# Kernel tuning notes

Hardware: AMD Instinct MI355X
Metric: run time of the kernel (lower is better)

Reference implementation:

```python
import jax, jax.numpy as jnp
import numpy as np

B = 1024
E = 200          # entity_dim (== relation_dim)
R = 200          # relation_dim
NE = 50000       # num_entities
NR = 400         # num_relations
OC = 32          # out_channels
FW = 9           # filt_w (filt_h = 1)
WP = E - FW + 1  # conv output width = 192
FC_IN = OC * WP  # 6144
EPS = 1e-5


def setup_inputs() -> dict:
    key = jax.random.key(0)
    ks = jax.random.split(key, 20)
    s = lambda n: 1.0 / np.sqrt(n)
    inp = {
        "e_s": jax.random.randint(ks[0], (B,), 0, NE, dtype=jnp.int32),
        "q_s": jax.random.randint(ks[1], (B,), 0, NR, dtype=jnp.int32),
        "e_c": jax.random.randint(ks[2], (B,), 0, NE, dtype=jnp.int32),
        "entity_emb": jax.random.normal(ks[3], (NE, E), jnp.float32) * 0.1,
        "relation_emb": jax.random.normal(ks[4], (NR, R), jnp.float32) * 0.1,
        "W1_w": jax.random.normal(ks[5], (E + R, R), jnp.float32) * s(E + R),
        "W1_b": jnp.zeros((R,), jnp.float32),
        "fc1_w": jax.random.normal(ks[6], (R, OC * FW), jnp.float32) * s(R),
        "fc1_b": jnp.zeros((OC * FW,), jnp.float32),
        "fc_w": jax.random.normal(ks[7], (FC_IN, E), jnp.float32) * s(FC_IN),
        "fc_b": jnp.zeros((E,), jnp.float32),
        "bn0_g": jnp.ones((1,), jnp.float32),
        "bn0_b": jnp.zeros((1,), jnp.float32),
        "bn0_m": jnp.zeros((1,), jnp.float32),
        "bn0_v": jnp.ones((1,), jnp.float32),
        "bn1_g": jnp.ones((OC,), jnp.float32),
        "bn1_b": jnp.zeros((OC,), jnp.float32),
        "bn1_m": jnp.zeros((OC,), jnp.float32),
        "bn1_v": jnp.ones((OC,), jnp.float32),
        "bn2_g": jnp.ones((E,), jnp.float32),
        "bn2_b": jnp.zeros((E,), jnp.float32),
        "bn2_m": jnp.zeros((E,), jnp.float32),
        "bn2_v": jnp.ones((E,), jnp.float32),
        "bias_b": jnp.zeros((NE,), jnp.float32),
    }
    return inp


def reference(e_s, q_s, e_c, entity_emb, relation_emb, W1_w, W1_b,
              fc1_w, fc1_b, fc_w, fc_b,
              bn0_g, bn0_b, bn0_m, bn0_v,
              bn1_g, bn1_b, bn1_m, bn1_v,
              bn2_g, bn2_b, bn2_m, bn2_v, bias_b):
    es = entity_emb[e_s]                      # [B,E]
    ec = entity_emb[e_c]                      # [B,E]
    r = relation_emb[q_s]                     # [B,R]
    # W1: Linear(E+R -> R); here R == E so e1 has width E
    e1 = jnp.concatenate([es, ec], -1) @ W1_w + W1_b          # [B,E]
    # bn0: single channel, inference mode
    x = (e1 - bn0_m) * (bn0_g / jnp.sqrt(bn0_v + EPS)) + bn0_b  # [B,E]
    # per-sample dynamic filters from fc1(r)
    k = (r @ fc1_w + fc1_b).reshape(B, OC, FW)                # [B,OC,FW]
    # grouped conv (groups=B) == per-sample 1D sliding dot products
    patches = jnp.stack([x[:, w:w + WP] for w in range(FW)], axis=-1)  # [B,WP,FW]
    conv = jnp.einsum('bpw,bow->bop', patches, k)             # [B,OC,WP]
    # bn1 over the OC channel, inference mode
    conv = (conv - bn1_m[:, None]) * (bn1_g / jnp.sqrt(bn1_v + EPS))[:, None] + bn1_b[:, None]
    flat = conv.reshape(B, FC_IN)                             # [B, OC*WP]
    h = flat @ fc_w + fc_b                                    # [B,E]
    h = (h - bn2_m) * (bn2_g / jnp.sqrt(bn2_v + EPS)) + bn2_b
    h = jax.nn.relu(h)
    logits = h @ entity_emb.T + bias_b                        # [B,NE]
    return jax.nn.sigmoid(logits)
```

## Files before the change

### kernel.cpp

```cpp
#include <hip/hip_runtime.h>

#define B_   1024
#define E_   200
#define NE_  50000
#define OC_  32
#define FW_  9
#define WP_  192
#define FCIN 6144
#define CATK 400
#define KDIM 288

typedef __attribute__((ext_vector_type(8))) short short8;
typedef __attribute__((ext_vector_type(4))) float floatx4;
typedef __attribute__((ext_vector_type(4))) unsigned short ushort4v;

static __device__ __forceinline__ float bf2f(unsigned short u) {
  return __uint_as_float(((unsigned)u) << 16);
}
static __device__ __forceinline__ unsigned short f2bf(float f) {
  unsigned u = __float_as_uint(f);
  u += 0x7FFFu + ((u >> 16) & 1u);
  return (unsigned short)(u >> 16);
}

#define PREP_CVT_BLKS   9766
#define PREP_GATH_BLKS  2400
#define PREP_W1_BLKS    28
#define PREP_FC1_BLKS   20
#define PREP_FCW_BLKS   384
#define PREP_R1 (PREP_CVT_BLKS)
#define PREP_R2 (PREP_R1 + PREP_GATH_BLKS)
#define PREP_R3 (PREP_R2 + PREP_W1_BLKS)
#define PREP_R4 (PREP_R3 + PREP_FC1_BLKS)
#define PREP_TOTAL (PREP_R4 + PREP_FCW_BLKS)

static __device__ __forceinline__ void transpose_region(
    const float* __restrict__ in, unsigned short* __restrict__ out,
    int N, int Npad, int K, int bx, int by,
    unsigned short (*lds)[65]) {
  int n0 = bx * 64, k0 = by * 64;
  int tx = threadIdx.x & 63, ty = threadIdx.x >> 6;
#pragma unroll
  for (int kk = 0; kk < 16; kk++) {
    int k = k0 + ty + 4 * kk;
    int n = n0 + tx;
    unsigned short v = 0;
    if (k < K && n < N) v = f2bf(in[(long)k * N + n]);
    lds[ty + 4 * kk][tx] = v;
  }
  __syncthreads();
#pragma unroll
  for (int kk = 0; kk < 16; kk++) {
    int k = k0 + tx;
    int n = n0 + ty + 4 * kk;
    if (n < Npad && k < K) out[(long)n * K + k] = lds[tx][ty + 4 * kk];
  }
}

__global__ __launch_bounds__(256) void k_prep(
    const float* __restrict__ ent, const float* __restrict__ rel,
    const int* __restrict__ e_s, const int* __restrict__ q_s, const int* __restrict__ e_c,
    const float* __restrict__ W1w, const float* __restrict__ fc1w, const float* __restrict__ fcw,
    unsigned short* __restrict__ entb, unsigned short* __restrict__ cat,
    unsigned short* __restrict__ rbuf, unsigned short* __restrict__ W1T,
    unsigned short* __restrict__ fc1T, unsigned short* __restrict__ fcwT) {
  __shared__ unsigned short lds[64][65];
  int blk = blockIdx.x, tid = threadIdx.x;
  if (blk < PREP_R1) {
    int i = blk * 256 + tid;
    if (i < NE_ * E_ / 4) {
      float4 v = ((const float4*)ent)[i];
      ushort4v o = {f2bf(v.x), f2bf(v.y), f2bf(v.z), f2bf(v.w)};
      ((ushort4v*)entb)[i] = o;
    }
  } else if (blk < PREP_R2) {
    int idx = (blk - PREP_R1) * 256 + tid;
    if (idx < B_ * CATK) {
      int s = idx / CATK, i = idx - s * CATK;
      int row = (i < E_) ? e_s[s] : e_c[s];
      int col = (i < E_) ? i : i - E_;
      cat[idx] = f2bf(ent[row * E_ + col]);
    } else {
      int j = idx - B_ * CATK;
      int s = j / E_, i = j - s * E_;
      rbuf[j] = f2bf(rel[q_s[s] * E_ + i]);
    }
  } else if (blk < PREP_R3) {
    int l = blk - PREP_R2;
    transpose_region(W1w, W1T, 200, 208, CATK, l % 4, l / 4, lds);
  } else if (blk < PREP_R4) {
    int l = blk - PREP_R3;
    transpose_region(fc1w, fc1T, 288, 288, E_, l % 5, l / 5, lds);
  } else {
    int l = blk - PREP_R4;
    transpose_region(fcw, fcwT, 200, 208, FCIN, l % 4, l / 4, lds);
  }
}

template<int NK, int RQ>
static __device__ __forceinline__ floatx4 gemm_64x16(
    const unsigned short* __restrict__ A, int lda,
    const unsigned short* __restrict__ Bt, int ldb, int m0, int n0) {
  int lane = threadIdx.x & 63;
  int wv   = threadIdx.x >> 6;
  int l16  = lane & 15, quad = lane >> 4;
  const unsigned short* ap = A  + (long)(m0 + 16 * wv + l16) * lda + quad * 8;
  const unsigned short* bp = Bt + (long)(n0 + l16) * ldb + quad * 8;
  floatx4 acc = {0.f, 0.f, 0.f, 0.f};
#pragma unroll 4
  for (int ks = 0; ks < NK; ks++) {
    short8 a = *(const short8*)(ap + ks * 32);
    short8 b = *(const short8*)(bp + ks * 32);
    acc = __builtin_amdgcn_mfma_f32_16x16x32_bf16(a, b, acc, 0, 0, 0);
  }
  if (RQ > 0) {
    short8 z = {0,0,0,0,0,0,0,0};
    short8 a = (quad < RQ) ? *(const short8*)(ap + NK * 32) : z;
    short8 b = (quad < RQ) ? *(const short8*)(bp + NK * 32) : z;
    acc = __builtin_amdgcn_mfma_f32_16x16x32_bf16(a, b, acc, 0, 0, 0);
  }
  return acc;
}

__global__ __launch_bounds__(256) void k_gemm_ek(
    const unsigned short* __restrict__ cat, const unsigned short* __restrict__ W1T,
    const float* __restrict__ W1b,
    const float* __restrict__ g0, const float* __restrict__ b0,
    const float* __restrict__ m0p, const float* __restrict__ v0,
    unsigned short* __restrict__ xbuf,
    const unsigned short* __restrict__ rbuf, const unsigned short* __restrict__ fc1T,
    const float* __restrict__ fc1b,
    const float* __restrict__ g1, const float* __restrict__ v1,
    unsigned short* __restrict__ kbuf) {
  int blk = blockIdx.x;
  int lane = threadIdx.x & 63, wv = threadIdx.x >> 6;
  int l16 = lane & 15, quad = lane >> 4;
  if (blk < 208) {
    int m0 = (blk & 15) * 64, n0 = (blk >> 4) * 16;
    floatx4 acc = gemm_64x16<12, 2>(cat, CATK, W1T, CATK, m0, n0);
    int j = n0 + l16;
    if (j < E_) {
      float s0  = g0[0] * rsqrtf(v0[0] + 1e-5f);
      float off = (W1b[j] - m0p[0]) * s0 + b0[0];
      int rbase = m0 + 16 * wv + quad * 4;
#pragma unroll
      for (int i = 0; i < 4; i++)
        xbuf[(rbase + i) * E_ + j] = f2bf(acc[i] * s0 + off);
    }
  } else {
    int l = blk - 208;
    int m0 = (l & 15) * 64, n0 = (l >> 4) * 16;
    floatx4 acc = gemm_64x16<6, 1>(rbuf, E_, fc1T, E_, m0, n0);
    int c = n0 + l16;
    int o = c / FW_;
    float s1 = g1[o] * rsqrtf(v1[o] + 1e-5f);
    float fb = fc1b[c];
    int rbase = m0 + 16 * wv + quad * 4;
#pragma unroll
    for (int i = 0; i < 4; i++)
      kbuf[(rbase + i) * KDIM + c] = f2bf((acc[i] + fb) * s1);
  }
}

__global__ __launch_bounds__(256) void k_conv(
    const unsigned short* __restrict__ xbuf, const unsigned short* __restrict__ kbuf,
    const float* __restrict__ g1, const float* __restrict__ b1,
    const float* __restrict__ m1, const float* __restrict__ v1,
    unsigned short* __restrict__ flat) {
  __shared__ float xs[E_];
  __shared__ float ks[KDIM];
  __shared__ float beta[OC_];
  int b = blockIdx.x, tid = threadIdx.x;
  if (tid < E_)  xs[tid] = bf2f(xbuf[b * E_ + tid]);
  for (int i = tid; i < KDIM; i += 256) ks[i] = bf2f(kbuf[b * KDIM + i]);
  if (tid < OC_) {
    float s = g1[tid] * rsqrtf(v1[tid] + 1e-5f);
    beta[tid] = b1[tid] - m1[tid] * s;
  }
  __syncthreads();
  int o = tid >> 3, pc = tid & 7;
  int p0 = pc * 24;
  float kw[FW_];
#pragma unroll
  for (int w = 0; w < FW_; w++) kw[w] = ks[o * FW_ + w];
  float xw[32];
#pragma unroll
  for (int q = 0; q < 8; q++) {
    float4 v = *(const float4*)&xs[p0 + 4 * q];
    xw[4 * q + 0] = v.x; xw[4 * q + 1] = v.y; xw[4 * q + 2] = v.z; xw[4 * q + 3] = v.w;
  }
  float bo = beta[o];
  unsigned short* fp = flat + b * FCIN + o * WP_ + p0;
#pragma unroll
  for (int j = 0; j < 24; j += 2) {
    float a0 = bo, a1 = bo;
#pragma unroll
    for (int w = 0; w < FW_; w++) {
      a0 += xw[j + w] * kw[w];
      a1 += xw[j + 1 + w] * kw[w];
    }
    unsigned pack = (unsigned)f2bf(a0) | ((unsigned)f2bf(a1) << 16);
    *(unsigned*)(fp + j) = pack;
  }
}

__global__ __launch_bounds__(256) void k_gemm_fc(
    const unsigned short* __restrict__ flat, const unsigned short* __restrict__ fcwT,
    float* __restrict__ partial) {
  int m0 = blockIdx.x * 64, n0 = blockIdx.y * 16, kc = blockIdx.z;
  int lane = threadIdx.x & 63, wv = threadIdx.x >> 6;
  int l16 = lane & 15, quad = lane >> 4;
  const unsigned short* ap = flat + (long)(m0 + 16 * wv + l16) * FCIN + kc * 768 + quad * 8;
  const unsigned short* bp = fcwT + (long)(n0 + l16) * FCIN + kc * 768 + quad * 8;
  floatx4 acc = {0.f, 0.f, 0.f, 0.f};
#pragma unroll 4
  for (int ks = 0; ks < 24; ks++) {
    short8 a = *(const short8*)(ap + ks * 32);
    short8 b = *(const short8*)(bp + ks * 32);
    acc = __builtin_amdgcn_mfma_f32_16x16x32_bf16(a, b, acc, 0, 0, 0);
  }
  int j = n0 + l16;
  int rbase = m0 + 16 * wv + quad * 4;
#pragma unroll
  for (int i = 0; i < 4; i++)
    partial[((long)kc * B_ + rbase + i) * 208 + j] = acc[i];
}

__global__ __launch_bounds__(256) void k_fc_epi(
    const float* __restrict__ partial, const float* __restrict__ fcb,
    const float* __restrict__ g2, const float* __restrict__ b2,
    const float* __restrict__ m2, const float* __restrict__ v2,
    unsigned short* __restrict__ hbuf) {
  int idx = blockIdx.x * 256 + threadIdx.x;
  if (idx >= B_ * E_) return;
  int m = idx / E_, j = idx - m * E_;
  float s = 0.f;
#pragma unroll
  for (int kc = 0; kc < 8; kc++) s += partial[((long)kc * B_ + m) * 208 + j];
  float s2 = g2[j] * rsqrtf(v2[j] + 1e-5f);
  float h = (s + fcb[j] - m2[j]) * s2 + b2[j];
  hbuf[idx] = f2bf(fmaxf(h, 0.f));
}

__global__ __launch_bounds__(512, 4) void k_gemm_out(
    const unsigned short* __restrict__ hbuf, const unsigned short* __restrict__ entb,
    const float* __restrict__ bias, float* __restrict__ out) {
  __shared__ __align__(16) unsigned short Blds[7 * 4 * 128 * 8];
  int g = blockIdx.x;
  int xcd = g & 7, local_ = g >> 3;
  int T = (xcd < 4 ? xcd * 196 : 784 + (xcd - 4) * 195) + local_;
  int mt = T & 3, nt = T >> 2;
  int m0 = mt * 256, n0 = nt * 128;
  int tid = threadIdx.x;

#pragma unroll
  for (int it = 0; it < 7; ++it) {
    int idx = it * 512 + tid;
    int ks = idx >> 9, qd = (idx >> 7) & 3, np = idx & 127;
    int col = 8 * (np & 15) + (np >> 4);
    int n = n0 + col;
    int kb = ks * 32 + qd * 8;
    short8 v = {0, 0, 0, 0, 0, 0, 0, 0};
    if (kb < 200 && n < NE_) v = *(const short8*)(entb + (long)n * E_ + kb);
    *(short8*)(Blds + idx * 8) = v;
  }
  __syncthreads();

  int lane = tid & 63, wv = tid >> 6;
  int l16 = lane & 15, quad = lane >> 4;
  const unsigned short* ap0 = hbuf + (long)(m0 + wv * 32 + l16) * E_ + quad * 8;
  const unsigned short* ap1 = ap0 + 16 * E_;

  floatx4 acc[16];
#pragma unroll
  for (int i = 0; i < 16; ++i) acc[i] = (floatx4){0.f, 0.f, 0.f, 0.f};

#pragma unroll
  for (int ks = 0; ks < 6; ++ks) {
    short8 a0 = *(const short8*)(ap0 + ks * 32);
    short8 a1 = *(const short8*)(ap1 + ks * 32);
    const unsigned short* bb = Blds + (ks * 4 + quad) * 1024 + l16 * 8;
#pragma unroll
    for (int nf = 0; nf < 8; ++nf) {
      short8 b = *(const short8*)(bb + nf * 128);
      acc[nf]     = __builtin_amdgcn_mfma_f32_16x16x32_bf16(a0, b, acc[nf], 0, 0, 0);
      acc[8 + nf] = __builtin_amdgcn_mfma_f32_16x16x32_bf16(a1, b, acc[8 + nf], 0, 0, 0);
    }
  }
  {
    short8 z = {0, 0, 0, 0, 0, 0, 0, 0};
    short8 a0 = (quad == 0) ? *(const short8*)(ap0 + 192) : z;
    short8 a1 = (quad == 0) ? *(const short8*)(ap1 + 192) : z;
    const unsigned short* bb = Blds + (24 + quad) * 1024 + l16 * 8;
#pragma unroll
    for (int nf = 0; nf < 8; ++nf) {
      short8 b = *(const short8*)(bb + nf * 128);
      acc[nf]     = __builtin_amdgcn_mfma_f32_16x16x32_bf16(a0, b, acc[nf], 0, 0, 0);
      acc[8 + nf] = __builtin_amdgcn_mfma_f32_16x16x32_bf16(a1, b, acc[8 + nf], 0, 0, 0);
    }
  }

  int nb = n0 + 8 * l16;
  if (nb >= NE_) return;
  float4 bi0 = *(const float4*)(bias + nb);
  float4 bi1 = *(const float4*)(bias + nb + 4);
#pragma unroll
  for (int mf = 0; mf < 2; ++mf) {
#pragma unroll
    for (int i = 0; i < 4; ++i) {
      int row = m0 + wv * 32 + mf * 16 + quad * 4 + i;
      float4 v0, v1;
      v0.x = 1.f / (1.f + __expf(-(acc[mf * 8 + 0][i] + bi0.x)));
      v0.y = 1.f / (1.f + __expf(-(acc[mf * 8 + 1][i] + bi0.y)));
      v0.z = 1.f / (1.f + __expf(-(acc[mf * 8 + 2][i] + bi0.z)));
      v0.w = 1.f / (1.f + __expf(-(acc[mf * 8 + 3][i] + bi0.w)));
      v1.x = 1.f / (1.f + __expf(-(acc[mf * 8 + 4][i] + bi1.x)));
      v1.y = 1.f / (1.f + __expf(-(acc[mf * 8 + 5][i] + bi1.y)));
      v1.z = 1.f / (1.f + __expf(-(acc[mf * 8 + 6][i] + bi1.z)));
      v1.w = 1.f / (1.f + __expf(-(acc[mf * 8 + 7][i] + bi1.w)));
      float* op = out + (long)row * NE_ + nb;
      *(float4*)op = v0;
      *(float4*)(op + 4) = v1;
    }
  }
}

extern "C" void kernel_launch(void* const* d_in, const int* in_sizes, int n_in,
                              void* d_out, int out_size, void* d_ws, size_t ws_size,
                              hipStream_t stream) {
  const int* e_s = (const int*)d_in[0];
  const int* q_s = (const int*)d_in[1];
  const int* e_c = (const int*)d_in[2];
  const float* ent  = (const float*)d_in[3];
  const float* rel  = (const float*)d_in[4];
  const float* W1w  = (const float*)d_in[5];
  const float* W1b  = (const float*)d_in[6];
  const float* fc1w = (const float*)d_in[7];
  const float* fc1b = (const float*)d_in[8];
  const float* fcw  = (const float*)d_in[9];
  const float* fcb  = (const float*)d_in[10];
  const float* g0 = (const float*)d_in[11];
  const float* b0 = (const float*)d_in[12];
  const float* m0 = (const float*)d_in[13];
  const float* v0 = (const float*)d_in[14];
  const float* g1 = (const float*)d_in[15];
  const float* b1 = (const float*)d_in[16];
  const float* m1 = (const float*)d_in[17];
  const float* v1 = (const float*)d_in[18];
  const float* g2 = (const float*)d_in[19];
  const float* b2 = (const float*)d_in[20];
  const float* m2 = (const float*)d_in[21];
  const float* v2 = (const float*)d_in[22];
  const float* bias = (const float*)d_in[23];
  float* out = (float*)d_out;

  char* w = (char*)d_ws;
  unsigned short* entb = (unsigned short*)(w + 0);
  unsigned short* cat  = (unsigned short*)(w + 20000256);
  unsigned short* rbuf = (unsigned short*)(w + 20819712);
  unsigned short* W1T  = (unsigned short*)(w + 21229568);
  unsigned short* fc1T = (unsigned short*)(w + 21396224);
  unsigned short* fcwT = (unsigned short*)(w + 21511680);
  unsigned short* xbuf = (unsigned short*)(w + 24067840);
  unsigned short* kbuf = (unsigned short*)(w + 24477696);
  unsigned short* flat = (unsigned short*)(w + 25067776);
  unsigned short* hbuf = (unsigned short*)(w + 37650944);
  float* partial       = (float*)(w + 38060800);

  k_prep<<<dim3(PREP_TOTAL), dim3(256), 0, stream>>>(
      ent, rel, e_s, q_s, e_c, W1w, fc1w, fcw, entb, cat, rbuf, W1T, fc1T, fcwT);
  k_gemm_ek<<<dim3(496), dim3(256), 0, stream>>>(
      cat, W1T, W1b, g0, b0, m0, v0, xbuf, rbuf, fc1T, fc1b, g1, v1, kbuf);
  k_conv<<<dim3(B_), dim3(256), 0, stream>>>(xbuf, kbuf, g1, b1, m1, v1, flat);
  k_gemm_fc<<<dim3(16, 13, 8), dim3(256), 0, stream>>>(flat, fcwT, partial);
  k_fc_epi<<<dim3((B_ * E_ + 255) / 256), dim3(256), 0, stream>>>(
      partial, fcb, g2, b2, m2, v2, hbuf);
  k_gemm_out<<<dim3(1564), dim3(512), 0, stream>>>(hbuf, entb, bias, out);
}
```

Baseline: 392.3 us.

## Fuse split-K FC reduction into GEMM, move entity conversion into conv kernel

```diff
diff --git a/kernel.cpp b/kernel.cpp
--- a/kernel.cpp
+++ b/kernel.cpp
@@ -23,13 +23,11 @@
   return (unsigned short)(u >> 16);
 }
 
-#define PREP_CVT_BLKS   9766
 #define PREP_GATH_BLKS  2400
 #define PREP_W1_BLKS    28
 #define PREP_FC1_BLKS   20
 #define PREP_FCW_BLKS   384
-#define PREP_R1 (PREP_CVT_BLKS)
-#define PREP_R2 (PREP_R1 + PREP_GATH_BLKS)
+#define PREP_R2 (PREP_GATH_BLKS)
 #define PREP_R3 (PREP_R2 + PREP_W1_BLKS)
 #define PREP_R4 (PREP_R3 + PREP_FC1_BLKS)
 #define PREP_TOTAL (PREP_R4 + PREP_FCW_BLKS)
@@ -61,20 +59,13 @@
     const float* __restrict__ ent, const float* __restrict__ rel,
     const int* __restrict__ e_s, const int* __restrict__ q_s, const int* __restrict__ e_c,
     const float* __restrict__ W1w, const float* __restrict__ fc1w, const float* __restrict__ fcw,
-    unsigned short* __restrict__ entb, unsigned short* __restrict__ cat,
-    unsigned short* __restrict__ rbuf, unsigned short* __restrict__ W1T,
-    unsigned short* __restrict__ fc1T, unsigned short* __restrict__ fcwT) {
+    unsigned short* __restrict__ cat, unsigned short* __restrict__ rbuf,
+    unsigned short* __restrict__ W1T, unsigned short* __restrict__ fc1T,
+    unsigned short* __restrict__ fcwT) {
   __shared__ unsigned short lds[64][65];
   int blk = blockIdx.x, tid = threadIdx.x;
-  if (blk < PREP_R1) {
-    int i = blk * 256 + tid;
-    if (i < NE_ * E_ / 4) {
-      float4 v = ((const float4*)ent)[i];
-      ushort4v o = {f2bf(v.x), f2bf(v.y), f2bf(v.z), f2bf(v.w)};
-      ((ushort4v*)entb)[i] = o;
-    }
-  } else if (blk < PREP_R2) {
-    int idx = (blk - PREP_R1) * 256 + tid;
+  if (blk < PREP_R2) {
+    int idx = blk * 256 + tid;
     if (idx < B_ * CATK) {
       int s = idx / CATK, i = idx - s * CATK;
       int row = (i < E_) ? e_s[s] : e_c[s];
@@ -162,15 +153,27 @@
   }
 }
 
+#define CVT_BLKS 9766
 __global__ __launch_bounds__(256) void k_conv(
     const unsigned short* __restrict__ xbuf, const unsigned short* __restrict__ kbuf,
     const float* __restrict__ g1, const float* __restrict__ b1,
     const float* __restrict__ m1, const float* __restrict__ v1,
-    unsigned short* __restrict__ flat) {
+    unsigned short* __restrict__ flat,
+    const float* __restrict__ ent, unsigned short* __restrict__ entb) {
   __shared__ float xs[E_];
   __shared__ float ks[KDIM];
   __shared__ float beta[OC_];
-  int b = blockIdx.x, tid = threadIdx.x;
+  int tid = threadIdx.x;
+  if (blockIdx.x >= B_) {
+    int i = (blockIdx.x - B_) * 256 + tid;
+    if (i < NE_ * E_ / 4) {
+      float4 v = ((const float4*)ent)[i];
+      ushort4v o = {f2bf(v.x), f2bf(v.y), f2bf(v.z), f2bf(v.w)};
+      __builtin_nontemporal_store(o, (ushort4v*)entb + i);
+    }
+    return;
+  }
+  int b = blockIdx.x;
   if (tid < E_)  xs[tid] = bf2f(xbuf[b * E_ + tid]);
   for (int i = tid; i < KDIM; i += 256) ks[i] = bf2f(kbuf[b * KDIM + i]);
   if (tid < OC_) {
@@ -204,42 +207,46 @@
   }
 }
 
-__global__ __launch_bounds__(256) void k_gemm_fc(
+__global__ __launch_bounds__(512) void k_gemm_fc2(
     const unsigned short* __restrict__ flat, const unsigned short* __restrict__ fcwT,
-    float* __restrict__ partial) {
-  int m0 = blockIdx.x * 64, n0 = blockIdx.y * 16, kc = blockIdx.z;
-  int lane = threadIdx.x & 63, wv = threadIdx.x >> 6;
-  int l16 = lane & 15, quad = lane >> 4;
-  const unsigned short* ap = flat + (long)(m0 + 16 * wv + l16) * FCIN + kc * 768 + quad * 8;
-  const unsigned short* bp = fcwT + (long)(n0 + l16) * FCIN + kc * 768 + quad * 8;
-  floatx4 acc = {0.f, 0.f, 0.f, 0.f};
-#pragma unroll 4
-  for (int ks = 0; ks < 24; ks++) {
-    short8 a = *(const short8*)(ap + ks * 32);
-    short8 b = *(const short8*)(bp + ks * 32);
-    acc = __builtin_amdgcn_mfma_f32_16x16x32_bf16(a, b, acc, 0, 0, 0);
-  }
-  int j = n0 + l16;
-  int rbase = m0 + 16 * wv + quad * 4;
-#pragma unroll
-  for (int i = 0; i < 4; i++)
-    partial[((long)kc * B_ + rbase + i) * 208 + j] = acc[i];
-}
-
-__global__ __launch_bounds__(256) void k_fc_epi(
-    const float* __restrict__ partial, const float* __restrict__ fcb,
+    const float* __restrict__ fcb,
     const float* __restrict__ g2, const float* __restrict__ b2,
     const float* __restrict__ m2, const float* __restrict__ v2,
     unsigned short* __restrict__ hbuf) {
-  int idx = blockIdx.x * 256 + threadIdx.x;
-  if (idx >= B_ * E_) return;
-  int m = idx / E_, j = idx - m * E_;
+  __shared__ float red[8][32][17];
+  int m0 = blockIdx.x * 32, n0 = blockIdx.y * 16;
+  int tid = threadIdx.x;
+  int lane = tid & 63, kc = tid >> 6;
+  int l16 = lane & 15, quad = lane >> 4;
+  const unsigned short* ap0 = flat + (long)(m0 + l16) * FCIN + kc * 768 + quad * 8;
+  const unsigned short* ap1 = ap0 + 16 * FCIN;
+  const unsigned short* bp  = fcwT + (long)(n0 + l16) * FCIN + kc * 768 + quad * 8;
+  floatx4 acc0 = {0.f, 0.f, 0.f, 0.f};
+  floatx4 acc1 = {0.f, 0.f, 0.f, 0.f};
+#pragma unroll 4
+  for (int ks = 0; ks < 24; ks++) {
+    short8 b  = *(const short8*)(bp  + ks * 32);
+    short8 a0 = *(const short8*)(ap0 + ks * 32);
+    short8 a1 = *(const short8*)(ap1 + ks * 32);
+    acc0 = __builtin_amdgcn_mfma_f32_16x16x32_bf16(a0, b, acc0, 0, 0, 0);
+    acc1 = __builtin_amdgcn_mfma_f32_16x16x32_bf16(a1, b, acc1, 0, 0, 0);
+  }
+#pragma unroll
+  for (int i = 0; i < 4; i++) {
+    red[kc][quad * 4 + i][l16]      = acc0[i];
+    red[kc][16 + quad * 4 + i][l16] = acc1[i];
+  }
+  __syncthreads();
+  int row = tid >> 4, col = tid & 15;
   float s = 0.f;
 #pragma unroll
-  for (int kc = 0; kc < 8; kc++) s += partial[((long)kc * B_ + m) * 208 + j];
-  float s2 = g2[j] * rsqrtf(v2[j] + 1e-5f);
-  float h = (s + fcb[j] - m2[j]) * s2 + b2[j];
-  hbuf[idx] = f2bf(fmaxf(h, 0.f));
+  for (int k2 = 0; k2 < 8; k2++) s += red[k2][row][col];
+  int j = n0 + col;
+  if (j < E_) {
+    float s2 = g2[j] * rsqrtf(v2[j] + 1e-5f);
+    float h = (s + fcb[j] - m2[j]) * s2 + b2[j];
+    hbuf[(m0 + row) * E_ + j] = f2bf(fmaxf(h, 0.f));
+  }
 }
 
 __global__ __launch_bounds__(512, 4) void k_gemm_out(
@@ -309,7 +316,7 @@
 #pragma unroll
     for (int i = 0; i < 4; ++i) {
       int row = m0 + wv * 32 + mf * 16 + quad * 4 + i;
-      float4 v0, v1;
+      floatx4 v0, v1;
       v0.x = 1.f / (1.f + __expf(-(acc[mf * 8 + 0][i] + bi0.x)));
       v0.y = 1.f / (1.f + __expf(-(acc[mf * 8 + 1][i] + bi0.y)));
       v0.z = 1.f / (1.f + __expf(-(acc[mf * 8 + 2][i] + bi0.z)));
@@ -319,8 +326,8 @@
       v1.z = 1.f / (1.f + __expf(-(acc[mf * 8 + 6][i] + bi1.z)));
       v1.w = 1.f / (1.f + __expf(-(acc[mf * 8 + 7][i] + bi1.w)));
       float* op = out + (long)row * NE_ + nb;
-      *(float4*)op = v0;
-      *(float4*)(op + 4) = v1;
+      __builtin_nontemporal_store(v0, (floatx4*)op);
+      __builtin_nontemporal_store(v1, (floatx4*)(op + 4));
     }
   }
 }
@@ -365,15 +372,14 @@
   unsigned short* kbuf = (unsigned short*)(w + 24477696);
   unsigned short* flat = (unsigned short*)(w + 25067776);
   unsigned short* hbuf = (unsigned short*)(w + 37650944);
-  float* partial       = (float*)(w + 38060800);
 
   k_prep<<<dim3(PREP_TOTAL), dim3(256), 0, stream>>>(
-      ent, rel, e_s, q_s, e_c, W1w, fc1w, fcw, entb, cat, rbuf, W1T, fc1T, fcwT);
+      ent, rel, e_s, q_s, e_c, W1w, fc1w, fcw, cat, rbuf, W1T, fc1T, fcwT);
   k_gemm_ek<<<dim3(496), dim3(256), 0, stream>>>(
       cat, W1T, W1b, g0, b0, m0, v0, xbuf, rbuf, fc1T, fc1b, g1, v1, kbuf);
-  k_conv<<<dim3(B_), dim3(256), 0, stream>>>(xbuf, kbuf, g1, b1, m1, v1, flat);
-  k_gemm_fc<<<dim3(16, 13, 8), dim3(256), 0, stream>>>(flat, fcwT, partial);
-  k_fc_epi<<<dim3((B_ * E_ + 255) / 256), dim3(256), 0, stream>>>(
-      partial, fcb, g2, b2, m2, v2, hbuf);
+  k_conv<<<dim3(B_ + CVT_BLKS), dim3(256), 0, stream>>>(
+      xbuf, kbuf, g1, b1, m1, v1, flat, ent, entb);
+  k_gemm_fc2<<<dim3(32, 13), dim3(512), 0, stream>>>(
+      flat, fcwT, fcb, g2, b2, m2, v2, hbuf);
   k_gemm_out<<<dim3(1564), dim3(512), 0, stream>>>(hbuf, entb, bias, out);
 }
```

After: 400.6 us. 1.02x slower.
